# Kernel optimization log

Measured on AMD Instinct MI355X. Metric: run time of the kernel, lower is better.

## Reference

```python
import jax, jax.numpy as jnp
import numpy as np

EMBED_DIM = 1024
Q_IN = 1024
KV_IN = 256
NUM_HEADS = 16
HEAD_DIM = EMBED_DIM // NUM_HEADS
SCALING = HEAD_DIM ** -0.5
BSZ, TGT, SRC = 8, 1024, 1024


def setup_inputs() -> dict:
    key = jax.random.key(0)
    ks = jax.random.split(key, 12)
    s = lambda fan_in: 1.0 / np.sqrt(fan_in)
    return {
        "hidden_states": jax.random.normal(ks[0], (BSZ, TGT, Q_IN), jnp.float32),
        "key_value_states": jax.random.normal(ks[1], (BSZ, SRC, KV_IN), jnp.float32),
        "attention_mask": jnp.zeros((BSZ, 1, TGT, SRC), jnp.float32),
        "layer_head_mask": jnp.ones((NUM_HEADS,), jnp.float32),
        "Wq": jax.random.normal(ks[2], (Q_IN, EMBED_DIM), jnp.float32) * s(Q_IN),
        "bq": jax.random.normal(ks[3], (EMBED_DIM,), jnp.float32) * 0.02,
        "Wk": jax.random.normal(ks[4], (KV_IN, EMBED_DIM), jnp.float32) * s(KV_IN),
        "bk": jax.random.normal(ks[5], (EMBED_DIM,), jnp.float32) * 0.02,
        "Wv": jax.random.normal(ks[6], (KV_IN, EMBED_DIM), jnp.float32) * s(KV_IN),
        "bv": jax.random.normal(ks[7], (EMBED_DIM,), jnp.float32) * 0.02,
        "Wo": jax.random.normal(ks[8], (EMBED_DIM, EMBED_DIM), jnp.float32) * s(EMBED_DIM),
        "bo": jax.random.normal(ks[9], (EMBED_DIM,), jnp.float32) * 0.02,
    }


def reference(hidden_states, key_value_states, attention_mask, layer_head_mask,
              Wq, bq, Wk, bk, Wv, bv, Wo, bo):
    b, t, _ = hidden_states.shape
    src = key_value_states.shape[1]
    # projections, split heads: [b, h, len, d]
    q = (hidden_states @ Wq + bq) * SCALING
    q = q.reshape(b, t, NUM_HEADS, HEAD_DIM).transpose(0, 2, 1, 3)
    k = (key_value_states @ Wk + bk).reshape(b, src, NUM_HEADS, HEAD_DIM).transpose(0, 2, 1, 3)
    v = (key_value_states @ Wv + bv).reshape(b, src, NUM_HEADS, HEAD_DIM).transpose(0, 2, 1, 3)
    # scores [b, h, t, src] + additive mask
    scores = jnp.einsum("bhtd,bhsd->bhts", q, k) + attention_mask
    probs = jax.nn.softmax(scores, axis=-1)
    # head mask multiply (dropout p=0 in eval)
    probs = probs * layer_head_mask[None, :, None, None]
    out = jnp.einsum("bhts,bhsd->bhtd", probs, v)
    out = out.transpose(0, 2, 1, 3).reshape(b, t, EMBED_DIM)
    return out @ Wo + bo
```

## Files before the change

### kernel.cpp

```cpp
#include <hip/hip_runtime.h>
#include <hip/hip_bf16.h>
#include <cstdint>

#define B_    8
#define T_    1024
#define S_    1024
#define E_    1024
#define NH_   16
#define HD_   64
#define KVIN_ 256
#define SCALE_ 0.125f

typedef __attribute__((ext_vector_type(8))) short bf16x8;
typedef __attribute__((ext_vector_type(4))) float f32x4;

__device__ __forceinline__ unsigned short f2bf(float x) {
  union { float f; unsigned u; } v; v.f = x;
  unsigned r = v.u + 0x7fffu + ((v.u >> 16) & 1u);
  return (unsigned short)(r >> 16);
}

__device__ __forceinline__ unsigned short f2bf_p(float x) {
  union { float f; unsigned u; } v; v.f = x;
  return (unsigned short)((v.u + 0x8000u) >> 16);
}

__device__ __forceinline__ void gl_lds16(const unsigned short* g, const unsigned short* l) {
  __builtin_amdgcn_global_load_lds(
      (const __attribute__((address_space(1))) void*)g,
      (__attribute__((address_space(3))) void*)l, 16, 0, 0);
}

__device__ __forceinline__ void cvt_body(const float* __restrict__ in,
                                         unsigned short* __restrict__ out, int blk, int tid) {
  int i = blk * 256 + tid;
  float4 v = ((const float4*)in)[i];
  ushort4 o;
  o.x = f2bf(v.x); o.y = f2bf(v.y); o.z = f2bf(v.z); o.w = f2bf(v.w);
  ((ushort4*)out)[i] = o;
}

__device__ __forceinline__ void tr_body(const float* __restrict__ W,
                                        unsigned short* __restrict__ Wt,
                                        int K, int N, int bx, int by, int tid) {
  __shared__ float t[32][33];
  int n0 = bx * 32, k0 = by * 32;
  int tx = tid & 31, ty = tid >> 5;
  #pragma unroll
  for (int r = 0; r < 32; r += 8)
    t[ty + r][tx] = W[(size_t)(k0 + ty + r) * N + n0 + tx];
  __syncthreads();
  #pragma unroll
  for (int r = 0; r < 32; r += 8)
    Wt[(size_t)(n0 + ty + r) * K + k0 + tx] = f2bf(t[tx][ty + r]);
}

__global__ __launch_bounds__(256) void k_prep(const float* __restrict__ hs, unsigned short* __restrict__ hsb,
                                              const float* __restrict__ kv, unsigned short* __restrict__ kvb,
                                              const float* __restrict__ Wq, unsigned short* __restrict__ Wqt,
                                              const float* __restrict__ Wk, unsigned short* __restrict__ Wkt,
                                              const float* __restrict__ Wv, unsigned short* __restrict__ Wvt,
                                              const float* __restrict__ Wo, unsigned short* __restrict__ Wot) {
  const int bid = blockIdx.x, tid = threadIdx.x;
  if (bid < 8192) { cvt_body(hs, hsb, bid, tid); return; }
  if (bid < 10240) { cvt_body(kv, kvb, bid - 8192, tid); return; }
  int id = bid - 10240;
  if (id < 1024)      tr_body(Wq, Wqt, 1024, 1024, id & 31, id >> 5, tid);
  else if (id < 1280) tr_body(Wk, Wkt, 256, 1024, (id - 1024) & 31, (id - 1024) >> 5, tid);
  else if (id < 1536) tr_body(Wv, Wvt, 256, 1024, (id - 1280) & 31, (id - 1280) >> 5, tid);
  else                tr_body(Wo, Wot, 1024, 1024, (id - 1536) & 31, (id - 1536) >> 5, tid);
}

__device__ __forceinline__ void gemm_body(const unsigned short* __restrict__ A, int lda,
                                          const unsigned short* __restrict__ Bt, int ldb,
                                          const float* __restrict__ bias,
                                          void* __restrict__ Cv, int K, int epi) {
  __shared__ unsigned short As[128 * 64];
  __shared__ unsigned short Bs[128 * 64];
  const int tid = threadIdx.x, lane = tid & 63, w = tid >> 6;
  const int quad = lane >> 4, lc = lane & 15;
  const int m0 = blockIdx.y * 128, n0 = blockIdx.x * 128;
  const int wm = (w >> 1) * 64, wn = (w & 1) * 64;

  f32x4 acc[4][4] = {};

  const int strow = w * 32 + (lane >> 3);
  const int stcol = (((lane & 7) ^ ((lane >> 3) & 7)) * 8);
  const unsigned short* Ag = A + (size_t)(m0 + strow) * lda + stcol;
  const unsigned short* Bg = Bt + (size_t)(n0 + strow) * ldb + stcol;

  for (int k0 = 0; k0 < K; k0 += 64) {
    __syncthreads();
    #pragma unroll
    for (int r = 0; r < 4; ++r) {
      gl_lds16(Ag + (size_t)r * 8 * lda + k0, As + (w * 4 + r) * 512);
      gl_lds16(Bg + (size_t)r * 8 * ldb + k0, Bs + (w * 4 + r) * 512);
    }
    __syncthreads();
    #pragma unroll
    for (int ks = 0; ks < 2; ++ks) {
      bf16x8 af[4], bfr[4];
      #pragma unroll
      for (int i = 0; i < 4; ++i) {
        af[i]  = *(const bf16x8*)(As + (wm + i * 16 + lc) * 64 + (((ks * 4 + quad) ^ (lc & 7)) * 8));
        bfr[i] = *(const bf16x8*)(Bs + (wn + i * 16 + lc) * 64 + (((ks * 4 + quad) ^ (lc & 7)) * 8));
      }
      #pragma unroll
      for (int mt = 0; mt < 4; ++mt)
        #pragma unroll
        for (int nt = 0; nt < 4; ++nt)
          acc[mt][nt] = __builtin_amdgcn_mfma_f32_16x16x32_bf16(af[mt], bfr[nt], acc[mt][nt], 0, 0, 0);
    }
  }

  #pragma unroll
  for (int mt = 0; mt < 4; ++mt) {
    #pragma unroll
    for (int nt = 0; nt < 4; ++nt) {
      const int n = n0 + wn + nt * 16 + lc;
      const float bn = bias[n];
      #pragma unroll
      for (int r = 0; r < 4; ++r) {
        const int m = m0 + wm + mt * 16 + quad * 4 + r;
        float v = acc[mt][nt][r] + bn;
        if (epi == 0)
          ((unsigned short*)Cv)[(size_t)m * E_ + n] = f2bf(v * SCALE_);
        else if (epi == 1)
          ((unsigned short*)Cv)[(size_t)m * E_ + n] = f2bf(v);
        else if (epi == 2)
          ((unsigned short*)Cv)[((size_t)((m >> 10) << 10) + n) * 1024 + (m & 1023)] = f2bf(v);
        else
          ((float*)Cv)[(size_t)m * E_ + n] = v;
      }
    }
  }
}

__global__ __launch_bounds__(256) void k_proj(const unsigned short* __restrict__ hsb,
                                              const unsigned short* __restrict__ kvb,
                                              const unsigned short* __restrict__ Wqt,
                                              const unsigned short* __restrict__ Wkt,
                                              const unsigned short* __restrict__ Wvt,
                                              const float* __restrict__ bq,
                                              const float* __restrict__ bk,
                                              const float* __restrict__ bv,
                                              unsigned short* __restrict__ Qb,
                                              unsigned short* __restrict__ Kb,
                                              unsigned short* __restrict__ Vtb) {
  const int z = blockIdx.z;
  const unsigned short* A = (z == 0) ? hsb : kvb;
  const unsigned short* Bt = (z == 0) ? Wqt : ((z == 1) ? Wkt : Wvt);
  const float* bias = (z == 0) ? bq : ((z == 1) ? bk : bv);
  void* Cv = (z == 0) ? (void*)Qb : ((z == 1) ? (void*)Kb : (void*)Vtb);
  const int K = (z == 0) ? 1024 : 256;
  gemm_body(A, K, Bt, K, bias, Cv, K, z);
}

__global__ __launch_bounds__(256) void k_oproj(const unsigned short* __restrict__ Ob,
                                               const unsigned short* __restrict__ Wot,
                                               const float* __restrict__ bo,
                                               float* __restrict__ out) {
  gemm_body(Ob, 1024, Wot, 1024, bo, (void*)out, 1024, 3);
}

__global__ __launch_bounds__(256, 4) void k_attn(const unsigned short* __restrict__ Q,
                                                 const unsigned short* __restrict__ Kg_,
                                                 const unsigned short* __restrict__ Vt,
                                                 const float* __restrict__ mask,
                                                 const float* __restrict__ lhm,
                                                 unsigned short* __restrict__ O) {
  __shared__ unsigned short Ks[64 * 64];
  __shared__ unsigned short Vs[64 * 64];
  __shared__ unsigned short Ps[4][32 * 72];

  const int tid = threadIdx.x, lane = tid & 63, w = tid >> 6;
  const int quad = lane >> 4, lc = lane & 15;
  const int bidx = blockIdx.x;
  const int qt = bidx & 7;
  const int h = (bidx >> 3) & 15;
  const int b = bidx >> 7;
  const int q0 = qt * 128 + w * 32;

  bf16x8 qf[2][2];
  #pragma unroll
  for (int mt = 0; mt < 2; ++mt) {
    const unsigned short* Qrow = Q + ((size_t)(b * 1024 + q0 + mt * 16 + lc)) * 1024 + h * 64 + quad * 8;
    qf[mt][0] = *(const bf16x8*)Qrow;
    qf[mt][1] = *(const bf16x8*)(Qrow + 32);
  }

  f32x4 oacc[2][4] = {};
  f32x4 lacc[2] = {};

  bf16x8 ones;
  #pragma unroll
  for (int i = 0; i < 8; ++i) ones[i] = (short)0x3F80;

  const int stsw = (((lane & 7) ^ ((lane >> 3) & 7)) * 8);
  const unsigned short* Kgs = Kg_ + ((size_t)(b * 1024) + w * 16 + (lane >> 3)) * 1024 + h * 64 + stsw;
  const unsigned short* Vgs = Vt + ((size_t)((b * 16 + h) * 64) + w * 16 + (lane >> 3)) * 1024 + stsw;
  const float* mg = mask + ((size_t)(b * 1024 + q0 + quad * 4)) * 1024 + lc;

  for (int s0 = 0; s0 < 1024; s0 += 64) {
    __syncthreads();
    #pragma unroll
    for (int r = 0; r < 2; ++r) {
      gl_lds16(Kgs + (size_t)(s0 + r * 8) * 1024, Ks + (w * 16 + r * 8) * 64);
      gl_lds16(Vgs + (size_t)(r * 8) * 1024 + s0, Vs + (w * 16 + r * 8) * 64);
    }
    __syncthreads();

    #pragma unroll
    for (int mt = 0; mt < 2; ++mt) {
      float mv[4][4];
      #pragma unroll
      for (int nt = 0; nt < 4; ++nt)
        #pragma unroll
        for (int r = 0; r < 4; ++r)
          mv[nt][r] = mg[(size_t)(mt * 16 + r) * 1024 + s0 + nt * 16];

      f32x4 sacc[4] = {};
      #pragma unroll
      for (int ks = 0; ks < 2; ++ks)
        #pragma unroll
        for (int nt = 0; nt < 4; ++nt) {
          bf16x8 kf = *(const bf16x8*)(Ks + (nt * 16 + lc) * 64 + (((ks * 4 + quad) ^ (lc & 7)) * 8));
          sacc[nt] = __builtin_amdgcn_mfma_f32_16x16x32_bf16(qf[mt][ks], kf, sacc[nt], 0, 0, 0);
        }

      #pragma unroll
      for (int nt = 0; nt < 4; ++nt)
        #pragma unroll
        for (int r = 0; r < 4; ++r) {
          float pv = __expf(sacc[nt][r] + mv[nt][r]);
          Ps[w][(mt * 16 + quad * 4 + r) * 72 + nt * 16 + lc] = f2bf_p(pv);
        }
    }

    #pragma unroll
    for (int ks = 0; ks < 2; ++ks) {
      bf16x8 pf0 = *(const bf16x8*)(&Ps[w][(0  + lc) * 72 + ks * 32 + quad * 8]);
      bf16x8 pf1 = *(const bf16x8*)(&Ps[w][(16 + lc) * 72 + ks * 32 + quad * 8]);
      lacc[0] = __builtin_amdgcn_mfma_f32_16x16x32_bf16(pf0, ones, lacc[0], 0, 0, 0);
      lacc[1] = __builtin_amdgcn_mfma_f32_16x16x32_bf16(pf1, ones, lacc[1], 0, 0, 0);
      #pragma unroll
      for (int nt = 0; nt < 4; ++nt) {
        bf16x8 vf = *(const bf16x8*)(Vs + (nt * 16 + lc) * 64 + (((ks * 4 + quad) ^ (lc & 7)) * 8));
        oacc[0][nt] = __builtin_amdgcn_mfma_f32_16x16x32_bf16(pf0, vf, oacc[0][nt], 0, 0, 0);
        oacc[1][nt] = __builtin_amdgcn_mfma_f32_16x16x32_bf16(pf1, vf, oacc[1][nt], 0, 0, 0);
      }
    }
  }

  const float hm = lhm[h];
  #pragma unroll
  for (int mt = 0; mt < 2; ++mt) {
    unsigned short* Og = O + ((size_t)(b * 1024 + q0 + mt * 16 + quad * 4)) * 1024 + h * 64 + lc;
    #pragma unroll
    for (int r = 0; r < 4; ++r) {
      float inv = hm / lacc[mt][r];
      #pragma unroll
      for (int nt = 0; nt < 4; ++nt)
        Og[(size_t)r * 1024 + nt * 16] = f2bf(oacc[mt][nt][r] * inv);
    }
  }
}

extern "C" void kernel_launch(void* const* d_in, const int* in_sizes, int n_in,
                              void* d_out, int out_size, void* d_ws, size_t ws_size,
                              hipStream_t stream) {
  (void)in_sizes; (void)n_in; (void)out_size; (void)ws_size;
  const float* hs   = (const float*)d_in[0];
  const float* kv   = (const float*)d_in[1];
  const float* mask = (const float*)d_in[2];
  const float* lhm  = (const float*)d_in[3];
  const float* Wq   = (const float*)d_in[4];
  const float* bq   = (const float*)d_in[5];
  const float* Wk   = (const float*)d_in[6];
  const float* bk   = (const float*)d_in[7];
  const float* Wv   = (const float*)d_in[8];
  const float* bv   = (const float*)d_in[9];
  const float* Wo   = (const float*)d_in[10];
  const float* bo   = (const float*)d_in[11];
  float* out = (float*)d_out;

  char* p = (char*)d_ws;
  auto alloc = [&](size_t bytes) { char* r = p; p += (bytes + 255) & ~(size_t)255; return r; };
  unsigned short* hsb = (unsigned short*)alloc((size_t)B_ * T_ * E_ * 2);
  unsigned short* kvb = (unsigned short*)alloc((size_t)B_ * S_ * KVIN_ * 2);
  unsigned short* Wqt = (unsigned short*)alloc((size_t)E_ * E_ * 2);
  unsigned short* Wkt = (unsigned short*)alloc((size_t)E_ * KVIN_ * 2);
  unsigned short* Wvt = (unsigned short*)alloc((size_t)E_ * KVIN_ * 2);
  unsigned short* Wot = (unsigned short*)alloc((size_t)E_ * E_ * 2);
  unsigned short* Qb  = (unsigned short*)alloc((size_t)B_ * T_ * E_ * 2);
  unsigned short* Kb  = (unsigned short*)alloc((size_t)B_ * S_ * E_ * 2);
  unsigned short* Vtb = (unsigned short*)alloc((size_t)B_ * S_ * E_ * 2);
  unsigned short* Ob  = (unsigned short*)alloc((size_t)B_ * T_ * E_ * 2);

  k_prep<<<12800, 256, 0, stream>>>(hs, hsb, kv, kvb, Wq, Wqt, Wk, Wkt, Wv, Wvt, Wo, Wot);

  k_proj<<<dim3(8, 64, 3), 256, 0, stream>>>(hsb, kvb, Wqt, Wkt, Wvt, bq, bk, bv, Qb, Kb, Vtb);

  k_attn<<<1024, 256, 0, stream>>>(Qb, Kb, Vtb, mask, lhm, Ob);

  k_oproj<<<dim3(8, 64), 256, 0, stream>>>(Ob, Wot, bo, out);
}
```

Measured before the change: 292.1 us.

## Double-buffer LDS tiles in GEMM and attention; pre-transpose mask to bf16

Both the projection GEMMs and the attention loop now use two LDS buffers. The next K/V or A/B tile is issued with global_load_lds before computing on the current one, which removes one barrier per iteration and overlaps loads with MFMA work. The prep kernel also transposes the additive attention mask into a bf16 [b, s, t] buffer, so attention reads narrower, vectorized mask values instead of strided fp32 ones. The trade-offs are extra prep traffic for the mask transpose, bf16 rounding of arbitrary mask values, doubled LDS use, and changed occupancy hints on the kernels.

```diff
diff --git a/kernel.cpp b/kernel.cpp
--- a/kernel.cpp
+++ b/kernel.cpp
@@ -13,26 +13,31 @@
 
 typedef __attribute__((ext_vector_type(8))) short bf16x8;
 typedef __attribute__((ext_vector_type(4))) float f32x4;
-
-__device__ __forceinline__ unsigned short f2bf(float x) {
+typedef unsigned short us;
+
+__device__ __forceinline__ us f2bf(float x) {
   union { float f; unsigned u; } v; v.f = x;
   unsigned r = v.u + 0x7fffu + ((v.u >> 16) & 1u);
-  return (unsigned short)(r >> 16);
-}
-
-__device__ __forceinline__ unsigned short f2bf_p(float x) {
+  return (us)(r >> 16);
+}
+
+__device__ __forceinline__ us f2bf_p(float x) {
   union { float f; unsigned u; } v; v.f = x;
-  return (unsigned short)((v.u + 0x8000u) >> 16);
-}
-
-__device__ __forceinline__ void gl_lds16(const unsigned short* g, const unsigned short* l) {
+  return (us)((v.u + 0x8000u) >> 16);
+}
+
+__device__ __forceinline__ float bf2f(us u) {
+  union { unsigned u32; float f; } x; x.u32 = (unsigned)u << 16; return x.f;
+}
+
+__device__ __forceinline__ void gl_lds16(const us* g, const us* l) {
   __builtin_amdgcn_global_load_lds(
       (const __attribute__((address_space(1))) void*)g,
       (__attribute__((address_space(3))) void*)l, 16, 0, 0);
 }
 
 __device__ __forceinline__ void cvt_body(const float* __restrict__ in,
-                                         unsigned short* __restrict__ out, int blk, int tid) {
+                                         us* __restrict__ out, int blk, int tid) {
   int i = blk * 256 + tid;
   float4 v = ((const float4*)in)[i];
   ushort4 o;
@@ -41,7 +46,7 @@
 }
 
 __device__ __forceinline__ void tr_body(const float* __restrict__ W,
-                                        unsigned short* __restrict__ Wt,
+                                        us* __restrict__ Wt,
                                         int K, int N, int bx, int by, int tid) {
   __shared__ float t[32][33];
   int n0 = bx * 32, k0 = by * 32;
@@ -55,28 +60,33 @@
     Wt[(size_t)(n0 + ty + r) * K + k0 + tx] = f2bf(t[tx][ty + r]);
 }
 
-__global__ __launch_bounds__(256) void k_prep(const float* __restrict__ hs, unsigned short* __restrict__ hsb,
-                                              const float* __restrict__ kv, unsigned short* __restrict__ kvb,
-                                              const float* __restrict__ Wq, unsigned short* __restrict__ Wqt,
-                                              const float* __restrict__ Wk, unsigned short* __restrict__ Wkt,
-                                              const float* __restrict__ Wv, unsigned short* __restrict__ Wvt,
-                                              const float* __restrict__ Wo, unsigned short* __restrict__ Wot) {
+__global__ __launch_bounds__(256) void k_prep(const float* __restrict__ hs, us* __restrict__ hsb,
+                                              const float* __restrict__ kv, us* __restrict__ kvb,
+                                              const float* __restrict__ Wq, us* __restrict__ Wqt,
+                                              const float* __restrict__ Wk, us* __restrict__ Wkt,
+                                              const float* __restrict__ Wv, us* __restrict__ Wvt,
+                                              const float* __restrict__ Wo, us* __restrict__ Wot,
+                                              const float* __restrict__ mask, us* __restrict__ mbT) {
   const int bid = blockIdx.x, tid = threadIdx.x;
   if (bid < 8192) { cvt_body(hs, hsb, bid, tid); return; }
   if (bid < 10240) { cvt_body(kv, kvb, bid - 8192, tid); return; }
   int id = bid - 10240;
-  if (id < 1024)      tr_body(Wq, Wqt, 1024, 1024, id & 31, id >> 5, tid);
-  else if (id < 1280) tr_body(Wk, Wkt, 256, 1024, (id - 1024) & 31, (id - 1024) >> 5, tid);
-  else if (id < 1536) tr_body(Wv, Wvt, 256, 1024, (id - 1280) & 31, (id - 1280) >> 5, tid);
-  else                tr_body(Wo, Wot, 1024, 1024, (id - 1536) & 31, (id - 1536) >> 5, tid);
-}
-
-__device__ __forceinline__ void gemm_body(const unsigned short* __restrict__ A, int lda,
-                                          const unsigned short* __restrict__ Bt, int ldb,
+  if (id < 1024)      { tr_body(Wq, Wqt, 1024, 1024, id & 31, id >> 5, tid); return; }
+  if (id < 1280)      { tr_body(Wk, Wkt, 256, 1024, (id - 1024) & 31, (id - 1024) >> 5, tid); return; }
+  if (id < 1536)      { tr_body(Wv, Wvt, 256, 1024, (id - 1280) & 31, (id - 1280) >> 5, tid); return; }
+  if (id < 2560)      { tr_body(Wo, Wot, 1024, 1024, (id - 1536) & 31, (id - 1536) >> 5, tid); return; }
+  int mid = id - 2560;
+  int bb = mid >> 10, t32 = mid & 1023;
+  tr_body(mask + (size_t)bb * 1024 * 1024, mbT + (size_t)bb * 1024 * 1024,
+          1024, 1024, t32 & 31, t32 >> 5, tid);
+}
+
+__device__ __forceinline__ void gemm_body(const us* __restrict__ A, int lda,
+                                          const us* __restrict__ Bt, int ldb,
                                           const float* __restrict__ bias,
                                           void* __restrict__ Cv, int K, int epi) {
-  __shared__ unsigned short As[128 * 64];
-  __shared__ unsigned short Bs[128 * 64];
+  __shared__ us As[2][128 * 64];
+  __shared__ us Bs[2][128 * 64];
   const int tid = threadIdx.x, lane = tid & 63, w = tid >> 6;
   const int quad = lane >> 4, lc = lane & 15;
   const int m0 = blockIdx.y * 128, n0 = blockIdx.x * 128;
@@ -86,24 +96,29 @@
 
   const int strow = w * 32 + (lane >> 3);
   const int stcol = (((lane & 7) ^ ((lane >> 3) & 7)) * 8);
-  const unsigned short* Ag = A + (size_t)(m0 + strow) * lda + stcol;
-  const unsigned short* Bg = Bt + (size_t)(n0 + strow) * ldb + stcol;
-
+  const us* Ag = A + (size_t)(m0 + strow) * lda + stcol;
+  const us* Bg = Bt + (size_t)(n0 + strow) * ldb + stcol;
+
+  auto stage = [&](int buf, int k0) {
+    #pragma unroll
+    for (int r = 0; r < 4; ++r) {
+      gl_lds16(Ag + (size_t)r * 8 * lda + k0, &As[buf][(w * 4 + r) * 512]);
+      gl_lds16(Bg + (size_t)r * 8 * ldb + k0, &Bs[buf][(w * 4 + r) * 512]);
+    }
+  };
+
+  stage(0, 0);
+  int cur = 0;
   for (int k0 = 0; k0 < K; k0 += 64) {
     __syncthreads();
-    #pragma unroll
-    for (int r = 0; r < 4; ++r) {
-      gl_lds16(Ag + (size_t)r * 8 * lda + k0, As + (w * 4 + r) * 512);
-      gl_lds16(Bg + (size_t)r * 8 * ldb + k0, Bs + (w * 4 + r) * 512);
-    }
-    __syncthreads();
+    if (k0 + 64 < K) stage(cur ^ 1, k0 + 64);
     #pragma unroll
     for (int ks = 0; ks < 2; ++ks) {
       bf16x8 af[4], bfr[4];
       #pragma unroll
       for (int i = 0; i < 4; ++i) {
-        af[i]  = *(const bf16x8*)(As + (wm + i * 16 + lc) * 64 + (((ks * 4 + quad) ^ (lc & 7)) * 8));
-        bfr[i] = *(const bf16x8*)(Bs + (wn + i * 16 + lc) * 64 + (((ks * 4 + quad) ^ (lc & 7)) * 8));
+        af[i]  = *(const bf16x8*)(&As[cur][(wm + i * 16 + lc) * 64 + (((ks * 4 + quad) ^ (lc & 7)) * 8)]);
+        bfr[i] = *(const bf16x8*)(&Bs[cur][(wn + i * 16 + lc) * 64 + (((ks * 4 + quad) ^ (lc & 7)) * 8)]);
       }
       #pragma unroll
       for (int mt = 0; mt < 4; ++mt)
@@ -111,6 +126,7 @@
         for (int nt = 0; nt < 4; ++nt)
           acc[mt][nt] = __builtin_amdgcn_mfma_f32_16x16x32_bf16(af[mt], bfr[nt], acc[mt][nt], 0, 0, 0);
     }
+    cur ^= 1;
   }
 
   #pragma unroll
@@ -124,11 +140,11 @@
         const int m = m0 + wm + mt * 16 + quad * 4 + r;
         float v = acc[mt][nt][r] + bn;
         if (epi == 0)
-          ((unsigned short*)Cv)[(size_t)m * E_ + n] = f2bf(v * SCALE_);
+          ((us*)Cv)[(size_t)m * E_ + n] = f2bf(v * SCALE_);
         else if (epi == 1)
-          ((unsigned short*)Cv)[(size_t)m * E_ + n] = f2bf(v);
+          ((us*)Cv)[(size_t)m * E_ + n] = f2bf(v);
         else if (epi == 2)
-          ((unsigned short*)Cv)[((size_t)((m >> 10) << 10) + n) * 1024 + (m & 1023)] = f2bf(v);
+          ((us*)Cv)[((size_t)((m >> 10) << 10) + n) * 1024 + (m & 1023)] = f2bf(v);
         else
           ((float*)Cv)[(size_t)m * E_ + n] = v;
       }
@@ -136,42 +152,42 @@
   }
 }
 
-__global__ __launch_bounds__(256) void k_proj(const unsigned short* __restrict__ hsb,
-                                              const unsigned short* __restrict__ kvb,
-                                              const unsigned short* __restrict__ Wqt,
-                                              const unsigned short* __restrict__ Wkt,
-                                              const unsigned short* __restrict__ Wvt,
-                                              const float* __restrict__ bq,
-                                              const float* __restrict__ bk,
-                                              const float* __restrict__ bv,
-                                              unsigned short* __restrict__ Qb,
-                                              unsigned short* __restrict__ Kb,
-                                              unsigned short* __restrict__ Vtb) {
+__global__ __launch_bounds__(256, 2) void k_proj(const us* __restrict__ hsb,
+                                                 const us* __restrict__ kvb,
+                                                 const us* __restrict__ Wqt,
+                                                 const us* __restrict__ Wkt,
+                                                 const us* __restrict__ Wvt,
+                                                 const float* __restrict__ bq,
+                                                 const float* __restrict__ bk,
+                                                 const float* __restrict__ bv,
+                                                 us* __restrict__ Qb,
+                                                 us* __restrict__ Kb,
+                                                 us* __restrict__ Vtb) {
   const int z = blockIdx.z;
-  const unsigned short* A = (z == 0) ? hsb : kvb;
-  const unsigned short* Bt = (z == 0) ? Wqt : ((z == 1) ? Wkt : Wvt);
+  const us* A = (z == 0) ? hsb : kvb;
+  const us* Bt = (z == 0) ? Wqt : ((z == 1) ? Wkt : Wvt);
   const float* bias = (z == 0) ? bq : ((z == 1) ? bk : bv);
   void* Cv = (z == 0) ? (void*)Qb : ((z == 1) ? (void*)Kb : (void*)Vtb);
   const int K = (z == 0) ? 1024 : 256;
   gemm_body(A, K, Bt, K, bias, Cv, K, z);
 }
 
-__global__ __launch_bounds__(256) void k_oproj(const unsigned short* __restrict__ Ob,
-                                               const unsigned short* __restrict__ Wot,
-                                               const float* __restrict__ bo,
-                                               float* __restrict__ out) {
+__global__ __launch_bounds__(256, 2) void k_oproj(const us* __restrict__ Ob,
+                                                  const us* __restrict__ Wot,
+                                                  const float* __restrict__ bo,
+                                                  float* __restrict__ out) {
   gemm_body(Ob, 1024, Wot, 1024, bo, (void*)out, 1024, 3);
 }
 
-__global__ __launch_bounds__(256, 4) void k_attn(const unsigned short* __restrict__ Q,
-                                                 const unsigned short* __restrict__ Kg_,
-                                                 const unsigned short* __restrict__ Vt,
-                                                 const float* __restrict__ mask,
+__global__ __launch_bounds__(256, 3) void k_attn(const us* __restrict__ Q,
+                                                 const us* __restrict__ Kg_,
+                                                 const us* __restrict__ Vt,
+                                                 const us* __restrict__ mbT,
                                                  const float* __restrict__ lhm,
-                                                 unsigned short* __restrict__ O) {
-  __shared__ unsigned short Ks[64 * 64];
-  __shared__ unsigned short Vs[64 * 64];
-  __shared__ unsigned short Ps[4][32 * 72];
+                                                 us* __restrict__ O) {
+  __shared__ us Ks[2][64 * 64];
+  __shared__ us Vs[2][64 * 64];
+  __shared__ us Ps[4][32 * 72];
 
   const int tid = threadIdx.x, lane = tid & 63, w = tid >> 6;
   const int quad = lane >> 4, lc = lane & 15;
@@ -184,7 +200,7 @@
   bf16x8 qf[2][2];
   #pragma unroll
   for (int mt = 0; mt < 2; ++mt) {
-    const unsigned short* Qrow = Q + ((size_t)(b * 1024 + q0 + mt * 16 + lc)) * 1024 + h * 64 + quad * 8;
+    const us* Qrow = Q + ((size_t)(b * 1024 + q0 + mt * 16 + lc)) * 1024 + h * 64 + quad * 8;
     qf[mt][0] = *(const bf16x8*)Qrow;
     qf[mt][1] = *(const bf16x8*)(Qrow + 32);
   }
@@ -197,44 +213,53 @@
   for (int i = 0; i < 8; ++i) ones[i] = (short)0x3F80;
 
   const int stsw = (((lane & 7) ^ ((lane >> 3) & 7)) * 8);
-  const unsigned short* Kgs = Kg_ + ((size_t)(b * 1024) + w * 16 + (lane >> 3)) * 1024 + h * 64 + stsw;
-  const unsigned short* Vgs = Vt + ((size_t)((b * 16 + h) * 64) + w * 16 + (lane >> 3)) * 1024 + stsw;
-  const float* mg = mask + ((size_t)(b * 1024 + q0 + quad * 4)) * 1024 + lc;
-
-  for (int s0 = 0; s0 < 1024; s0 += 64) {
+  const us* Kgs = Kg_ + ((size_t)(b * 1024) + w * 16 + (lane >> 3)) * 1024 + h * 64 + stsw;
+  const us* Vgs = Vt + ((size_t)((b * 16 + h) * 64) + w * 16 + (lane >> 3)) * 1024 + stsw;
+  const us* mbase = mbT + (size_t)b * 1024 * 1024;
+
+  auto stage = [&](int buf, int s0) {
+    #pragma unroll
+    for (int r = 0; r < 2; ++r) {
+      gl_lds16(Kgs + (size_t)(s0 + r * 8) * 1024, &Ks[buf][(w * 16 + r * 8) * 64]);
+      gl_lds16(Vgs + (size_t)(r * 8) * 1024 + s0, &Vs[buf][(w * 16 + r * 8) * 64]);
+    }
+  };
+
+  stage(0, 0);
+  int cur = 0;
+  for (int it = 0; it < 16; ++it) {
+    const int s0 = it * 64;
     __syncthreads();
-    #pragma unroll
-    for (int r = 0; r < 2; ++r) {
-      gl_lds16(Kgs + (size_t)(s0 + r * 8) * 1024, Ks + (w * 16 + r * 8) * 64);
-      gl_lds16(Vgs + (size_t)(r * 8) * 1024 + s0, Vs + (w * 16 + r * 8) * 64);
-    }
-    __syncthreads();
+    if (it < 15) stage(cur ^ 1, s0 + 64);
+
+    ushort4 mvv[2][4];
+    #pragma unroll
+    for (int mt = 0; mt < 2; ++mt)
+      #pragma unroll
+      for (int nt = 0; nt < 4; ++nt)
+        mvv[mt][nt] = *(const ushort4*)(mbase + (size_t)(s0 + nt * 16 + lc) * 1024 +
+                                        q0 + mt * 16 + quad * 4);
 
     #pragma unroll
     for (int mt = 0; mt < 2; ++mt) {
-      float mv[4][4];
-      #pragma unroll
-      for (int nt = 0; nt < 4; ++nt)
-        #pragma unroll
-        for (int r = 0; r < 4; ++r)
-          mv[nt][r] = mg[(size_t)(mt * 16 + r) * 1024 + s0 + nt * 16];
-
       f32x4 sacc[4] = {};
       #pragma unroll
       for (int ks = 0; ks < 2; ++ks)
         #pragma unroll
         for (int nt = 0; nt < 4; ++nt) {
-          bf16x8 kf = *(const bf16x8*)(Ks + (nt * 16 + lc) * 64 + (((ks * 4 + quad) ^ (lc & 7)) * 8));
+          bf16x8 kf = *(const bf16x8*)(&Ks[cur][(nt * 16 + lc) * 64 + (((ks * 4 + quad) ^ (lc & 7)) * 8)]);
           sacc[nt] = __builtin_amdgcn_mfma_f32_16x16x32_bf16(qf[mt][ks], kf, sacc[nt], 0, 0, 0);
         }
 
       #pragma unroll
-      for (int nt = 0; nt < 4; ++nt)
+      for (int nt = 0; nt < 4; ++nt) {
+        const us* mu = (const us*)&mvv[mt][nt];
         #pragma unroll
         for (int r = 0; r < 4; ++r) {
-          float pv = __expf(sacc[nt][r] + mv[nt][r]);
+          float pv = __expf(sacc[nt][r] + bf2f(mu[r]));
           Ps[w][(mt * 16 + quad * 4 + r) * 72 + nt * 16 + lc] = f2bf_p(pv);
         }
+      }
     }
 
     #pragma unroll
@@ -245,17 +270,18 @@
       lacc[1] = __builtin_amdgcn_mfma_f32_16x16x32_bf16(pf1, ones, lacc[1], 0, 0, 0);
       #pragma unroll
       for (int nt = 0; nt < 4; ++nt) {
-        bf16x8 vf = *(const bf16x8*)(Vs + (nt * 16 + lc) * 64 + (((ks * 4 + quad) ^ (lc & 7)) * 8));
+        bf16x8 vf = *(const bf16x8*)(&Vs[cur][(nt * 16 + lc) * 64 + (((ks * 4 + quad) ^ (lc & 7)) * 8)]);
         oacc[0][nt] = __builtin_amdgcn_mfma_f32_16x16x32_bf16(pf0, vf, oacc[0][nt], 0, 0, 0);
         oacc[1][nt] = __builtin_amdgcn_mfma_f32_16x16x32_bf16(pf1, vf, oacc[1][nt], 0, 0, 0);
       }
     }
+    cur ^= 1;
   }
 
   const float hm = lhm[h];
   #pragma unroll
   for (int mt = 0; mt < 2; ++mt) {
-    unsigned short* Og = O + ((size_t)(b * 1024 + q0 + mt * 16 + quad * 4)) * 1024 + h * 64 + lc;
+    us* Og = O + ((size_t)(b * 1024 + q0 + mt * 16 + quad * 4)) * 1024 + h * 64 + lc;
     #pragma unroll
     for (int r = 0; r < 4; ++r) {
       float inv = hm / lacc[mt][r];
@@ -286,22 +312,24 @@
 
   char* p = (char*)d_ws;
   auto alloc = [&](size_t bytes) { char* r = p; p += (bytes + 255) & ~(size_t)255; return r; };
-  unsigned short* hsb = (unsigned short*)alloc((size_t)B_ * T_ * E_ * 2);
-  unsigned short* kvb = (unsigned short*)alloc((size_t)B_ * S_ * KVIN_ * 2);
-  unsigned short* Wqt = (unsigned short*)alloc((size_t)E_ * E_ * 2);
-  unsigned short* Wkt = (unsigned short*)alloc((size_t)E_ * KVIN_ * 2);
-  unsigned short* Wvt = (unsigned short*)alloc((size_t)E_ * KVIN_ * 2);
-  unsigned short* Wot = (unsigned short*)alloc((size_t)E_ * E_ * 2);
-  unsigned short* Qb  = (unsigned short*)alloc((size_t)B_ * T_ * E_ * 2);
-  unsigned short* Kb  = (unsigned short*)alloc((size_t)B_ * S_ * E_ * 2);
-  unsigned short* Vtb = (unsigned short*)alloc((size_t)B_ * S_ * E_ * 2);
-  unsigned short* Ob  = (unsigned short*)alloc((size_t)B_ * T_ * E_ * 2);
-
-  k_prep<<<12800, 256, 0, stream>>>(hs, hsb, kv, kvb, Wq, Wqt, Wk, Wkt, Wv, Wvt, Wo, Wot);
+  us* hsb = (us*)alloc((size_t)B_ * T_ * E_ * 2);
+  us* kvb = (us*)alloc((size_t)B_ * S_ * KVIN_ * 2);
+  us* Wqt = (us*)alloc((size_t)E_ * E_ * 2);
+  us* Wkt = (us*)alloc((size_t)E_ * KVIN_ * 2);
+  us* Wvt = (us*)alloc((size_t)E_ * KVIN_ * 2);
+  us* Wot = (us*)alloc((size_t)E_ * E_ * 2);
+  us* Qb  = (us*)alloc((size_t)B_ * T_ * E_ * 2);
+  us* Kb  = (us*)alloc((size_t)B_ * S_ * E_ * 2);
+  us* Vtb = (us*)alloc((size_t)B_ * S_ * E_ * 2);
+  us* Ob  = (us*)alloc((size_t)B_ * T_ * E_ * 2);
+  us* mbT = (us*)alloc((size_t)B_ * T_ * S_ * 2);
+
+  k_prep<<<20992, 256, 0, stream>>>(hs, hsb, kv, kvb, Wq, Wqt, Wk, Wkt, Wv, Wvt, Wo, Wot,
+                                    mask, mbT);
 
   k_proj<<<dim3(8, 64, 3), 256, 0, stream>>>(hsb, kvb, Wqt, Wkt, Wvt, bq, bk, bv, Qb, Kb, Vtb);
 
-  k_attn<<<1024, 256, 0, stream>>>(Qb, Kb, Vtb, mask, lhm, Ob);
+  k_attn<<<1024, 256, 0, stream>>>(Qb, Kb, Vtb, mbT, lhm, Ob);
 
   k_oproj<<<dim3(8, 64), 256, 0, stream>>>(Ob, Wot, bo, out);
 }
```

Result: slower. 329.7 us (+12.9%).
